# Kernel tuning notes

Measured on AMD Instinct MI355X. Metric: run time of the kernel, lower is better.

The kernel has to match this reference:

```python
import jax, jax.numpy as jnp
import numpy as np

DIM, H, DH = 1024, 16, 64
SCALE = 1.0 / np.sqrt(DH)


def setup_inputs() -> dict:
    key = jax.random.key(0)
    ks = jax.random.split(key, 16)
    B, S = 2, 2048
    glorot = jax.nn.initializers.glorot_uniform()
    def qkv(k):
        return glorot(k, (DIM, H, DH), jnp.float32)
    inp = {
        "x": jax.random.normal(ks[0], (B, S, DIM), jnp.float32),
        "layer_idx": 3,
        "lambda_param": jnp.full((1,), 0.8, jnp.float32),
    }
    for i, br in enumerate(["1", "2"]):
        base = 1 + i * 4
        inp[f"Wq{br}"] = qkv(ks[base])
        inp[f"Wk{br}"] = qkv(ks[base + 1])
        inp[f"Wv{br}"] = qkv(ks[base + 2])
        inp[f"Wo{br}"] = glorot(ks[base + 3], (H, DH, DIM), jnp.float32).reshape(H, DH, DIM)
        inp[f"bq{br}"] = jnp.zeros((H, DH), jnp.float32)
        inp[f"bk{br}"] = jnp.zeros((H, DH), jnp.float32)
        inp[f"bv{br}"] = jnp.zeros((H, DH), jnp.float32)
        inp[f"bo{br}"] = jnp.zeros((DIM,), jnp.float32)
    inp["Wp"] = glorot(ks[9], (DIM, DIM), jnp.float32)
    inp["bp"] = jnp.zeros((DIM,), jnp.float32)
    return inp


def _mha(x, Wq, bq, Wk, bk, Wv, bv, Wo, bo):
    # x: [B,S,D]; per-head projections as in keras.layers.MultiHeadAttention
    q = jnp.einsum("bsd,dhk->bshk", x, Wq) + bq   # [B,S,H,Dh]
    k = jnp.einsum("bsd,dhk->bshk", x, Wk) + bk
    v = jnp.einsum("bsd,dhk->bshk", x, Wv) + bv
    scores = jnp.einsum("bqhd,bkhd->bhqk", q, k) * SCALE  # [B,H,S,S]
    attn = jax.nn.softmax(scores, axis=-1)
    o = jnp.einsum("bhqk,bkhd->bqhd", attn, v)            # [B,S,H,Dh]
    return jnp.einsum("bqhd,hdo->bqo", o, Wo) + bo        # [B,S,D]


def _get_lambda(lambda_param, layer_idx):
    lf = jnp.asarray(layer_idx, jnp.float32)
    exp_term = jnp.exp(-0.3 * jnp.maximum(lf - 1.0, 0.0))
    init = 0.8 - 0.6 * exp_term
    return jnp.clip(init * lambda_param[0], 0.1, 0.9)


def reference(x, layer_idx, lambda_param,
              Wq1, bq1, Wk1, bk1, Wv1, bv1, Wo1, bo1,
              Wq2, bq2, Wk2, bk2, Wv2, bv2, Wo2, bo2,
              Wp, bp):
    a1 = _mha(x, Wq1, bq1, Wk1, bk1, Wv1, bv1, Wo1, bo1)
    a2 = _mha(x, Wq2, bq2, Wk2, bk2, Wv2, bv2, Wo2, bo2)
    lam = _get_lambda(lambda_param, layer_idx)
    diff = a1 - lam * a2
    return diff @ Wp + bp  # dropout is identity at inference
```

## Files before the change

### kernel.cpp

```cpp
#include <hip/hip_runtime.h>
#include <math.h>

typedef unsigned short u16;
typedef __attribute__((ext_vector_type(8))) short bf16x8;
typedef __attribute__((ext_vector_type(4))) float f32x4;
typedef __attribute__((ext_vector_type(4))) unsigned short u16x4;
typedef __attribute__((ext_vector_type(8))) unsigned short u16x8;

constexpr int Sq = 2048, Dm = 1024, Hh = 16, DH = 64;
constexpr int NT = 4096;
constexpr float SEXP = 0.125f * 1.44269504f;

#if __has_builtin(__builtin_amdgcn_exp2f)
#define EXP2(x) __builtin_amdgcn_exp2f(x)
#else
#define EXP2(x) exp2f(x)
#endif

__device__ __forceinline__ u16 f2bf(float f) {
    unsigned u = __float_as_uint(f);
    return (u16)((u + 0x7FFF + ((u >> 16) & 1)) >> 16);
}

__device__ __forceinline__ void async16(u16* lds, const u16* g) {
    __builtin_amdgcn_global_load_lds(
        (const __attribute__((address_space(1))) unsigned int*)g,
        (__attribute__((address_space(3))) unsigned int*)lds, 16, 0, 0);
}

__device__ __forceinline__ float lam_of(const int* lidx, const float* lamp) {
    float lf = (float)lidx[0];
    float init = 0.8f - 0.6f * __expf(-0.3f * fmaxf(lf - 1.0f, 0.0f));
    return fminf(fmaxf(init * lamp[0], 0.1f), 0.9f);
}

__device__ __forceinline__ void gemm_tile_128(
    const u16* __restrict__ A, const u16* __restrict__ Bt, int K,
    int aRow0, int bCol0, u16* As, u16* Bs, f32x4 acc[4][4])
{
    const int tid = threadIdx.x;
    const int w = tid >> 6, lane = tid & 63;
    const int ln = lane & 15, quad = lane >> 4;
    const int wm = (w >> 1) * 64, wn = (w & 1) * 64;
    const int l3 = lane & 7, lr8 = lane >> 3;

    for (int kt = 0; kt < K; kt += 64) {
        __syncthreads();
        #pragma unroll
        for (int c0 = 0; c0 < 4; ++c0) {
            int c = w * 4 + c0;
            int lr = c * 8 + lr8;
            int sc = l3 ^ (lr & 7);
            async16(As + c * 512, A + (size_t)(aRow0 + lr) * K + kt + sc * 8);
            async16(Bs + c * 512, Bt + (size_t)(bCol0 + lr) * K + kt + sc * 8);
        }
        __syncthreads();
        #pragma unroll
        for (int kc = 0; kc < 2; ++kc) {
            bf16x8 af[4], bfr[4];
            #pragma unroll
            for (int mt = 0; mt < 4; ++mt)
                af[mt] = *(const bf16x8*)(As + (wm + mt * 16 + ln) * 64 +
                                          (((kc * 4 + quad) ^ (ln & 7)) * 8));
            #pragma unroll
            for (int nt = 0; nt < 4; ++nt)
                bfr[nt] = *(const bf16x8*)(Bs + (wn + nt * 16 + ln) * 64 +
                                           (((kc * 4 + quad) ^ (ln & 7)) * 8));
            #pragma unroll
            for (int mt = 0; mt < 4; ++mt)
                #pragma unroll
                for (int nt = 0; nt < 4; ++nt)
                    acc[mt][nt] = __builtin_amdgcn_mfma_f32_16x16x32_bf16(
                        af[mt], bfr[nt], acc[mt][nt], 0, 0, 0);
        }
    }
}

__device__ __forceinline__ void gemm_tile_64(
    const u16* __restrict__ A, const u16* __restrict__ Bt, int K,
    int aRow0, int bCol0, u16* As, u16* Bs, f32x4 acc[2][4])
{
    const int tid = threadIdx.x;
    const int w = tid >> 6, lane = tid & 63;
    const int ln = lane & 15, quad = lane >> 4;
    const int wm = (w >> 1) * 32, wn = (w & 1) * 64;
    const int l3 = lane & 7, lr8 = lane >> 3;

    for (int kt = 0; kt < K; kt += 64) {
        __syncthreads();
        #pragma unroll
        for (int c0 = 0; c0 < 2; ++c0) {
            int c = w * 2 + c0;
            int lr = c * 8 + lr8;
            int sc = l3 ^ (lr & 7);
            async16(As + c * 512, A + (size_t)(aRow0 + lr) * K + kt + sc * 8);
        }
        #pragma unroll
        for (int c0 = 0; c0 < 4; ++c0) {
            int c = w * 4 + c0;
            int lr = c * 8 + lr8;
            int sc = l3 ^ (lr & 7);
            async16(Bs + c * 512, Bt + (size_t)(bCol0 + lr) * K + kt + sc * 8);
        }
        __syncthreads();
        #pragma unroll
        for (int kc = 0; kc < 2; ++kc) {
            bf16x8 af[2], bfr[4];
            #pragma unroll
            for (int mt = 0; mt < 2; ++mt)
                af[mt] = *(const bf16x8*)(As + (wm + mt * 16 + ln) * 64 +
                                          (((kc * 4 + quad) ^ (ln & 7)) * 8));
            #pragma unroll
            for (int nt = 0; nt < 4; ++nt)
                bfr[nt] = *(const bf16x8*)(Bs + (wn + nt * 16 + ln) * 64 +
                                           (((kc * 4 + quad) ^ (ln & 7)) * 8));
            #pragma unroll
            for (int mt = 0; mt < 2; ++mt)
                #pragma unroll
                for (int nt = 0; nt < 4; ++nt)
                    acc[mt][nt] = __builtin_amdgcn_mfma_f32_16x16x32_bf16(
                        af[mt], bfr[nt], acc[mt][nt], 0, 0, 0);
        }
    }
}

__global__ __launch_bounds__(256)
void convert_x(const float* __restrict__ x, u16* __restrict__ xb)
{
    int i = (blockIdx.x * 256 + threadIdx.x) * 4;
    float4 v = *(const float4*)(x + i);
    u16x4 o;
    o.x = f2bf(v.x); o.y = f2bf(v.y); o.z = f2bf(v.z); o.w = f2bf(v.w);
    *(u16x4*)(xb + i) = o;
}

struct TcP { const float* src[7]; u16* dst[7]; };

__global__ __launch_bounds__(256)
void wconv(TcP p)
{
    __shared__ float t[64][65];
    const int z = blockIdx.z;
    const float* __restrict__ src = p.src[z];
    u16* __restrict__ dst = p.dst[z];
    const int kb = blockIdx.y * 64, nb = blockIdx.x * 64;
    const int tid = threadIdx.x;
    {
        int r = tid >> 2, cs = (tid & 3) * 16;
        #pragma unroll
        for (int j4 = 0; j4 < 16; j4 += 4) {
            float4 v = *(const float4*)&src[(size_t)(kb + r) * 1024 + nb + cs + j4];
            t[r][cs + j4 + 0] = v.x; t[r][cs + j4 + 1] = v.y;
            t[r][cs + j4 + 2] = v.z; t[r][cs + j4 + 3] = v.w;
        }
    }
    __syncthreads();
    {
        int n = tid >> 2, ks = (tid & 3) * 16;
        u16x8 a, b;
        #pragma unroll
        for (int j = 0; j < 8; ++j) a[j] = f2bf(t[ks + j][n]);
        #pragma unroll
        for (int j = 0; j < 8; ++j) b[j] = f2bf(t[ks + 8 + j][n]);
        u16* o = &dst[(size_t)(nb + n) * 1024 + kb + ks];
        *(u16x8*)o = a;
        *(u16x8*)(o + 8) = b;
    }
}

__global__ __launch_bounds__(256)
void woconv(const float* __restrict__ Wo1, const float* __restrict__ Wo2,
            const float* __restrict__ bo1, const float* __restrict__ bo2,
            const int* __restrict__ lidx, const float* __restrict__ lamp,
            u16* __restrict__ Acat)
{
    const float lam = lam_of(lidx, lamp);
    int i = (blockIdx.x * 256 + threadIdx.x) * 4;
    float4 v;
    if (i < 1048576) {
        v = *(const float4*)(Wo1 + i);
    } else if (i < 2097152) {
        v = *(const float4*)(Wo2 + (i - 1048576));
        v.x *= -lam; v.y *= -lam; v.z *= -lam; v.w *= -lam;
    } else {
        int c = i - 2097152;
        float4 a = *(const float4*)(bo1 + c);
        float4 b = *(const float4*)(bo2 + c);
        v.x = a.x - lam * b.x; v.y = a.y - lam * b.y;
        v.z = a.z - lam * b.z; v.w = a.w - lam * b.w;
    }
    u16x4 o;
    o.x = f2bf(v.x); o.y = f2bf(v.y); o.z = f2bf(v.z); o.w = f2bf(v.w);
    *(u16x4*)(Acat + i) = o;
}

__global__ __launch_bounds__(256, 4)
void wfull_mfma(const u16* __restrict__ Acat, const u16* __restrict__ Wpt,
                const float* __restrict__ bp, u16* __restrict__ Wfull_bt,
                float* __restrict__ bfull)
{
    __shared__ u16 As[64 * 64], Bs[128 * 64];
    const int aRow0 = blockIdx.y * 64, nCol0 = blockIdx.x * 128;
    f32x4 acc[2][4] = {};
    gemm_tile_64(Acat, Wpt, 1024, aRow0, nCol0, As, Bs, acc);

    const int tid = threadIdx.x, w = tid >> 6, lane = tid & 63;
    const int ln = lane & 15, quad = lane >> 4;
    const int wm = (w >> 1) * 32, wn = (w & 1) * 64;
    #pragma unroll
    for (int mt = 0; mt < 2; ++mt) {
        #pragma unroll
        for (int nt = 0; nt < 4; ++nt) {
            int gn = nCol0 + wn + nt * 16 + ln;
            #pragma unroll
            for (int r = 0; r < 4; ++r) {
                int gm = aRow0 + wm + mt * 16 + quad * 4 + r;
                if (gm < 2048)
                    Wfull_bt[(size_t)gn * 2048 + gm] = f2bf(acc[mt][nt][r]);
                else if (gm == 2048)
                    bfull[gn] = acc[mt][nt][r] + bp[gn];
            }
        }
    }
}

struct QkvP { const u16* Wt[6]; const float* bias[6]; u16* out[6]; };

__global__ __launch_bounds__(256, 3)
void qkv_mfma(const u16* __restrict__ xb, QkvP p)
{
    __shared__ u16 As[128 * 64], Bs[128 * 64];
    const int z = blockIdx.z;
    const int type = (z < 3) ? z : z - 3;
    const int aRow0 = blockIdx.y * 128, nCol0 = blockIdx.x * 128;
    f32x4 acc[4][4] = {};
    gemm_tile_128(xb, p.Wt[z], 1024, aRow0, nCol0, As, Bs, acc);

    const float* __restrict__ bias = p.bias[z];
    u16* __restrict__ out = p.out[z];
    const int tid = threadIdx.x, w = tid >> 6, lane = tid & 63;
    const int ln = lane & 15, quad = lane >> 4;
    const int wm = (w >> 1) * 64, wn = (w & 1) * 64;
    #pragma unroll
    for (int mt = 0; mt < 4; ++mt) {
        #pragma unroll
        for (int nt = 0; nt < 4; ++nt) {
            int gn = nCol0 + wn + nt * 16 + ln;
            int h = gn >> 6, dh = gn & 63;
            float bv = bias[gn];
            #pragma unroll
            for (int r = 0; r < 4; ++r) {
                int gm = aRow0 + wm + mt * 16 + quad * 4 + r;
                int b = gm >> 11, s = gm & (Sq - 1);
                size_t bh = (size_t)(b * Hh + h);
                float fv = acc[mt][nt][r] + bv;
                size_t idx;
                u16 val;
                if (type == 0) {
                    val = f2bf(fv * SEXP);
                    idx = bh * 131072 + (size_t)s * 64 + dh;
                } else if (type == 1) {
                    val = f2bf(fv);
                    idx = bh * 131072 + (size_t)(s >> 5) * 2048 +
                          (size_t)((dh >> 5) * 2 + ((s >> 4) & 1)) * 512 +
                          (size_t)(((dh >> 3) & 3) * 16 + (s & 15)) * 8 + (dh & 7);
                } else {
                    val = f2bf(fv);
                    int kidx = ((s & 15) * 2) + ((s >> 4) & 1);
                    idx = bh * 131072 + (size_t)(s >> 5) * 2048 +
                          (size_t)(dh >> 4) * 512 +
                          (size_t)((kidx >> 3) * 16 + (dh & 15)) * 8 + (kidx & 7);
                }
                out[idx] = val;
            }
        }
    }
}

__global__ __launch_bounds__(256, 4)
void attn_mfma(const u16* __restrict__ q1, const u16* __restrict__ kf1,
               const u16* __restrict__ vf1,
               const u16* __restrict__ q2, const u16* __restrict__ kf2,
               const u16* __restrict__ vf2, u16* __restrict__ ocat)
{
    __shared__ __align__(16) char smem[10240];

    const int bh = blockIdx.x, qblk = blockIdx.y, br = blockIdx.z;
    const u16* __restrict__ q  = br ? q2  : q1;
    const u16* __restrict__ kf = br ? kf2 : kf1;
    const u16* __restrict__ vf = br ? vf2 : vf1;

    const int tid = threadIdx.x, w = tid >> 6, lane = tid & 63;
    const int ln = lane & 15, quad = lane >> 4;
    char* Pbase = smem + w * 2560;

    const u16* qbase = q + (size_t)bh * 131072 +
                       (size_t)(qblk * 128 + w * 32) * 64;
    bf16x8 qf[2][2];
    #pragma unroll
    for (int mt = 0; mt < 2; ++mt)
        #pragma unroll
        for (int kc = 0; kc < 2; ++kc)
            qf[mt][kc] = *(const bf16x8*)(qbase + (mt * 16 + ln) * 64 +
                                          kc * 32 + quad * 8);

    bf16x8 ones;
    #pragma unroll
    for (int j = 0; j < 8; ++j) ones[j] = (short)0x3F80;
    const f32x4 zero4 = {0.f, 0.f, 0.f, 0.f};

    f32x4 oacc[2][4] = {};
    f32x4 lacc[2] = {};

    const u16* kbase = kf + (size_t)bh * 131072 + lane * 8;
    const u16* vbase = vf + (size_t)bh * 131072 + lane * 8;

    for (int it = 0; it < 32; ++it) {
        #pragma unroll
        for (int u = 0; u < 2; ++u) {
            const int kt = it * 2 + u;
            const u16* kp = kbase + (size_t)kt * 2048;
            const u16* vp = vbase + (size_t)kt * 2048;

            bf16x8 kfr[2][2];
            #pragma unroll
            for (int kc = 0; kc < 2; ++kc)
                #pragma unroll
                for (int nt = 0; nt < 2; ++nt)
                    kfr[nt][kc] = *(const bf16x8*)(kp + (kc * 2 + nt) * 512);

            f32x4 sacc[2][2];
            #pragma unroll
            for (int mt = 0; mt < 2; ++mt)
                #pragma unroll
                for (int nt = 0; nt < 2; ++nt)
                    sacc[mt][nt] = __builtin_amdgcn_mfma_f32_16x16x32_bf16(
                        qf[mt][0], kfr[nt][0], zero4, 0, 0, 0);
            #pragma unroll
            for (int mt = 0; mt < 2; ++mt)
                #pragma unroll
                for (int nt = 0; nt < 2; ++nt)
                    sacc[mt][nt] = __builtin_amdgcn_mfma_f32_16x16x32_bf16(
                        qf[mt][1], kfr[nt][1], sacc[mt][nt], 0, 0, 0);

            #pragma unroll
            for (int mt = 0; mt < 2; ++mt) {
                #pragma unroll
                for (int r = 0; r < 4; ++r) {
                    float p0 = EXP2(sacc[mt][0][r]);
                    float p1 = EXP2(sacc[mt][1][r]);
                    unsigned a  = __float_as_uint(p0) + 0x8000u;
                    unsigned b2 = __float_as_uint(p1) + 0x8000u;
                    unsigned pk = __builtin_amdgcn_perm(b2, a, 0x07060302);
                    int row = mt * 16 + quad * 4 + r;
                    *(unsigned*)(Pbase + row * 80 + (((ln >> 2) ^ r) << 4) +
                                 ((ln & 3) << 2)) = pk;
                }
            }

            bf16x8 vfr[4];
            #pragma unroll
            for (int dt = 0; dt < 4; ++dt)
                vfr[dt] = *(const bf16x8*)(vp + dt * 512);

            #pragma unroll
            for (int mt = 0; mt < 2; ++mt) {
                bf16x8 pf = *(const bf16x8*)(Pbase + (mt * 16 + ln) * 80 +
                                             ((quad ^ (ln & 3)) << 4));
                lacc[mt] = __builtin_amdgcn_mfma_f32_16x16x32_bf16(
                    pf, ones, lacc[mt], 0, 0, 0);
                #pragma unroll
                for (int dt = 0; dt < 4; ++dt)
                    oacc[mt][dt] = __builtin_amdgcn_mfma_f32_16x16x32_bf16(
                        pf, vfr[dt], oacc[mt][dt], 0, 0, 0);
            }
        }
        __builtin_amdgcn_s_barrier();
    }

    const int b = bh >> 4, h = bh & 15;
    #pragma unroll
    for (int mt = 0; mt < 2; ++mt) {
        #pragma unroll
        for (int r = 0; r < 4; ++r) {
            float inv = 1.0f / lacc[mt][r];
            int s = qblk * 128 + w * 32 + mt * 16 + quad * 4 + r;
            size_t rowb = (size_t)(b * Sq + s) * 2048 + br * 1024 + h * 64;
            #pragma unroll
            for (int dt = 0; dt < 4; ++dt)
                ocat[rowb + dt * 16 + ln] = f2bf(oacc[mt][dt][r] * inv);
        }
    }
}

__global__ __launch_bounds__(256, 4)
void out_mfma(const u16* __restrict__ ocat, const u16* __restrict__ Wfull_bt,
              const float* __restrict__ bfull, float* __restrict__ outb)
{
    __shared__ u16 As[64 * 64], Bs[128 * 64];
    const int aRow0 = blockIdx.y * 64, nCol0 = blockIdx.x * 128;
    f32x4 acc[2][4] = {};
    gemm_tile_64(ocat, Wfull_bt, 2048, aRow0, nCol0, As, Bs, acc);

    const int tid = threadIdx.x, w = tid >> 6, lane = tid & 63;
    const int ln = lane & 15, quad = lane >> 4;
    const int wm = (w >> 1) * 32, wn = (w & 1) * 64;
    #pragma unroll
    for (int mt = 0; mt < 2; ++mt) {
        #pragma unroll
        for (int nt = 0; nt < 4; ++nt) {
            int gn = nCol0 + wn + nt * 16 + ln;
            float bv = bfull[gn];
            #pragma unroll
            for (int r = 0; r < 4; ++r) {
                int gm = aRow0 + wm + mt * 16 + quad * 4 + r;
                outb[(size_t)gm * 1024 + gn] = acc[mt][nt][r] + bv;
            }
        }
    }
}

extern "C" void kernel_launch(void* const* d_in, const int* in_sizes, int n_in,
                              void* d_out, int out_size, void* d_ws, size_t ws_size,
                              hipStream_t stream)
{
    const float* x    = (const float*)d_in[0];
    const int*   lidx = (const int*)  d_in[1];
    const float* lamp = (const float*)d_in[2];
    const float* Wq1  = (const float*)d_in[3];
    const float* Wk1  = (const float*)d_in[4];
    const float* Wv1  = (const float*)d_in[5];
    const float* Wo1  = (const float*)d_in[6];
    const float* bq1  = (const float*)d_in[7];
    const float* bk1  = (const float*)d_in[8];
    const float* bv1  = (const float*)d_in[9];
    const float* bo1  = (const float*)d_in[10];
    const float* Wq2  = (const float*)d_in[11];
    const float* Wk2  = (const float*)d_in[12];
    const float* Wv2  = (const float*)d_in[13];
    const float* Wo2  = (const float*)d_in[14];
    const float* bq2  = (const float*)d_in[15];
    const float* bk2  = (const float*)d_in[16];
    const float* bv2  = (const float*)d_in[17];
    const float* bo2  = (const float*)d_in[18];
    const float* Wp   = (const float*)d_in[19];
    const float* bp   = (const float*)d_in[20];

    char* wsb = (char*)d_ws;
    const size_t MB = 1 << 20;
    u16* xb    = (u16*)(wsb + 0 * MB);
    u16* Wt0   = (u16*)(wsb + 8 * MB);
    u16* Wpt   = (u16*)(wsb + 20 * MB);
    u16* Acat  = (u16*)(wsb + 22 * MB);
    u16* Wfull = (u16*)(wsb + 27 * MB);
    float* bfull = (float*)(wsb + 31 * MB);
    u16* qb1   = (u16*)(wsb + 32 * MB);
    u16* kb1   = (u16*)(wsb + 40 * MB);
    u16* vb1   = (u16*)(wsb + 48 * MB);
    u16* qb2   = (u16*)(wsb + 56 * MB);
    u16* kb2   = (u16*)(wsb + 64 * MB);
    u16* vb2   = (u16*)(wsb + 72 * MB);
    u16* ocat  = (u16*)(wsb + 80 * MB);

    convert_x<<<dim3(NT * Dm / 1024), dim3(256), 0, stream>>>(x, xb);

    TcP tp;
    const float* wsrc[7] = {Wq1, Wk1, Wv1, Wq2, Wk2, Wv2, Wp};
    for (int i = 0; i < 7; ++i) tp.src[i] = wsrc[i];
    for (int i = 0; i < 6; ++i) tp.dst[i] = Wt0 + (size_t)i * 1024 * 1024;
    tp.dst[6] = Wpt;
    wconv<<<dim3(16, 16, 7), dim3(256), 0, stream>>>(tp);

    woconv<<<dim3(2049), dim3(256), 0, stream>>>(
        Wo1, Wo2, bo1, bo2, lidx, lamp, Acat);

    wfull_mfma<<<dim3(8, 33), dim3(256), 0, stream>>>(
        Acat, Wpt, bp, Wfull, bfull);

    QkvP qp;
    qp.Wt[0] = Wt0 + 0 * 1048576; qp.bias[0] = bq1; qp.out[0] = qb1;
    qp.Wt[1] = Wt0 + 1 * 1048576; qp.bias[1] = bk1; qp.out[1] = kb1;
    qp.Wt[2] = Wt0 + 2 * 1048576; qp.bias[2] = bv1; qp.out[2] = vb1;
    qp.Wt[3] = Wt0 + 3 * 1048576; qp.bias[3] = bq2; qp.out[3] = qb2;
    qp.Wt[4] = Wt0 + 4 * 1048576; qp.bias[4] = bk2; qp.out[4] = kb2;
    qp.Wt[5] = Wt0 + 5 * 1048576; qp.bias[5] = bv2; qp.out[5] = vb2;
    qkv_mfma<<<dim3(8, 32, 6), dim3(256), 0, stream>>>(xb, qp);

    attn_mfma<<<dim3(32, 16, 2), dim3(256), 0, stream>>>(
        qb1, kb1, vb1, qb2, kb2, vb2, ocat);

    out_mfma<<<dim3(8, 64), dim3(256), 0, stream>>>(
        ocat, Wfull, bfull, (float*)d_out);
}
```

Baseline: 330.5 us.

## Double-buffer GEMM tiles, merge prep and GEMM launches, raise MFMA priority

The 128-wide GEMM tile loop now double-buffers its LDS tiles, issuing async loads for the next K-slice while the current one is multiplied. The three prep kernels are merged into one launch, and the Wfull and QKV GEMMs into a single gemms launch selected by blockIdx.z. The attention kernel wraps its MFMA sections in s_setprio(1)/s_setprio(0). These changes aim to cut launch overhead and load latency, at the cost of more LDS per block (64KB shared buffer, launch bounds of 2) and some idle blocks in the merged grid.

```diff
diff --git a/kernel.cpp b/kernel.cpp
--- a/kernel.cpp
+++ b/kernel.cpp
@@ -44,27 +44,43 @@
     const int wm = (w >> 1) * 64, wn = (w & 1) * 64;
     const int l3 = lane & 7, lr8 = lane >> 3;
 
+    #pragma unroll
+    for (int c0 = 0; c0 < 4; ++c0) {
+        int c = w * 4 + c0;
+        int lr = c * 8 + lr8;
+        int sc = l3 ^ (lr & 7);
+        async16(As + c * 512, A + (size_t)(aRow0 + lr) * K + sc * 8);
+        async16(Bs + c * 512, Bt + (size_t)(bCol0 + lr) * K + sc * 8);
+    }
+    __syncthreads();
+
+    int cur = 0;
     for (int kt = 0; kt < K; kt += 64) {
-        __syncthreads();
-        #pragma unroll
-        for (int c0 = 0; c0 < 4; ++c0) {
-            int c = w * 4 + c0;
-            int lr = c * 8 + lr8;
-            int sc = l3 ^ (lr & 7);
-            async16(As + c * 512, A + (size_t)(aRow0 + lr) * K + kt + sc * 8);
-            async16(Bs + c * 512, Bt + (size_t)(bCol0 + lr) * K + kt + sc * 8);
-        }
-        __syncthreads();
+        const int ktn = kt + 64;
+        if (ktn < K) {
+            u16* Asn = As + (cur ^ 1) * 8192;
+            u16* Bsn = Bs + (cur ^ 1) * 8192;
+            #pragma unroll
+            for (int c0 = 0; c0 < 4; ++c0) {
+                int c = w * 4 + c0;
+                int lr = c * 8 + lr8;
+                int sc = l3 ^ (lr & 7);
+                async16(Asn + c * 512, A + (size_t)(aRow0 + lr) * K + ktn + sc * 8);
+                async16(Bsn + c * 512, Bt + (size_t)(bCol0 + lr) * K + ktn + sc * 8);
+            }
+        }
+        const u16* Asc = As + cur * 8192;
+        const u16* Bsc = Bs + cur * 8192;
         #pragma unroll
         for (int kc = 0; kc < 2; ++kc) {
             bf16x8 af[4], bfr[4];
             #pragma unroll
             for (int mt = 0; mt < 4; ++mt)
-                af[mt] = *(const bf16x8*)(As + (wm + mt * 16 + ln) * 64 +
+                af[mt] = *(const bf16x8*)(Asc + (wm + mt * 16 + ln) * 64 +
                                           (((kc * 4 + quad) ^ (ln & 7)) * 8));
             #pragma unroll
             for (int nt = 0; nt < 4; ++nt)
-                bfr[nt] = *(const bf16x8*)(Bs + (wn + nt * 16 + ln) * 64 +
+                bfr[nt] = *(const bf16x8*)(Bsc + (wn + nt * 16 + ln) * 64 +
                                            (((kc * 4 + quad) ^ (ln & 7)) * 8));
             #pragma unroll
             for (int mt = 0; mt < 4; ++mt)
@@ -73,6 +89,8 @@
                     acc[mt][nt] = __builtin_amdgcn_mfma_f32_16x16x32_bf16(
                         af[mt], bfr[nt], acc[mt][nt], 0, 0, 0);
         }
+        __syncthreads();
+        cur ^= 1;
     }
 }
 
@@ -124,122 +142,130 @@
     }
 }
 
+struct PrepP {
+    const float* x; u16* xb;
+    const float* wsrc[7]; u16* wdst[7];
+    const float* Wo1; const float* Wo2;
+    const float* bo1; const float* bo2;
+    const int* lidx; const float* lamp;
+    u16* Acat;
+};
+
 __global__ __launch_bounds__(256)
-void convert_x(const float* __restrict__ x, u16* __restrict__ xb)
-{
-    int i = (blockIdx.x * 256 + threadIdx.x) * 4;
-    float4 v = *(const float4*)(x + i);
-    u16x4 o;
-    o.x = f2bf(v.x); o.y = f2bf(v.y); o.z = f2bf(v.z); o.w = f2bf(v.w);
-    *(u16x4*)(xb + i) = o;
-}
-
-struct TcP { const float* src[7]; u16* dst[7]; };
-
-__global__ __launch_bounds__(256)
-void wconv(TcP p)
+void prep(PrepP p)
 {
     __shared__ float t[64][65];
+    int b = blockIdx.x;
+    const int tid = threadIdx.x;
+
+    if (b < 4096) {
+        int i = (b * 256 + tid) * 4;
+        float4 v = *(const float4*)(p.x + i);
+        u16x4 o;
+        o.x = f2bf(v.x); o.y = f2bf(v.y); o.z = f2bf(v.z); o.w = f2bf(v.w);
+        *(u16x4*)(p.xb + i) = o;
+        return;
+    }
+    b -= 4096;
+    if (b < 1792) {
+        int z = b >> 8;
+        int rem = b & 255;
+        const float* __restrict__ src = p.wsrc[z];
+        u16* __restrict__ dst = p.wdst[z];
+        const int kb = (rem >> 4) * 64, nb = (rem & 15) * 64;
+        {
+            int r = tid >> 2, cs = (tid & 3) * 16;
+            #pragma unroll
+            for (int j4 = 0; j4 < 16; j4 += 4) {
+                float4 v = *(const float4*)&src[(size_t)(kb + r) * 1024 + nb + cs + j4];
+                t[r][cs + j4 + 0] = v.x; t[r][cs + j4 + 1] = v.y;
+                t[r][cs + j4 + 2] = v.z; t[r][cs + j4 + 3] = v.w;
+            }
+        }
+        __syncthreads();
+        {
+            int n = tid >> 2, ks = (tid & 3) * 16;
+            u16x8 a2, b2;
+            #pragma unroll
+            for (int j = 0; j < 8; ++j) a2[j] = f2bf(t[ks + j][n]);
+            #pragma unroll
+            for (int j = 0; j < 8; ++j) b2[j] = f2bf(t[ks + 8 + j][n]);
+            u16* o = &dst[(size_t)(nb + n) * 1024 + kb + ks];
+            *(u16x8*)o = a2;
+            *(u16x8*)(o + 8) = b2;
+        }
+        return;
+    }
+    b -= 1792;
+    {
+        const float lam = lam_of(p.lidx, p.lamp);
+        int i = (b * 256 + tid) * 4;
+        float4 v;
+        if (i < 1048576) {
+            v = *(const float4*)(p.Wo1 + i);
+        } else if (i < 2097152) {
+            v = *(const float4*)(p.Wo2 + (i - 1048576));
+            v.x *= -lam; v.y *= -lam; v.z *= -lam; v.w *= -lam;
+        } else {
+            int c = i - 2097152;
+            float4 a = *(const float4*)(p.bo1 + c);
+            float4 b2 = *(const float4*)(p.bo2 + c);
+            v.x = a.x - lam * b2.x; v.y = a.y - lam * b2.y;
+            v.z = a.z - lam * b2.z; v.w = a.w - lam * b2.w;
+        }
+        u16x4 o;
+        o.x = f2bf(v.x); o.y = f2bf(v.y); o.z = f2bf(v.z); o.w = f2bf(v.w);
+        *(u16x4*)(p.Acat + i) = o;
+    }
+}
+
+struct GemmP {
+    const u16* xb;
+    const u16* Wt[6]; const float* bias[6]; u16* out[6];
+    const u16* Acat; const u16* Wpt; const float* bp;
+    u16* Wfull_bt; float* bfull;
+};
+
+__global__ __launch_bounds__(256, 2)
+void gemms(GemmP p)
+{
+    __shared__ u16 smem[32768];
     const int z = blockIdx.z;
-    const float* __restrict__ src = p.src[z];
-    u16* __restrict__ dst = p.dst[z];
-    const int kb = blockIdx.y * 64, nb = blockIdx.x * 64;
-    const int tid = threadIdx.x;
-    {
-        int r = tid >> 2, cs = (tid & 3) * 16;
-        #pragma unroll
-        for (int j4 = 0; j4 < 16; j4 += 4) {
-            float4 v = *(const float4*)&src[(size_t)(kb + r) * 1024 + nb + cs + j4];
-            t[r][cs + j4 + 0] = v.x; t[r][cs + j4 + 1] = v.y;
-            t[r][cs + j4 + 2] = v.z; t[r][cs + j4 + 3] = v.w;
-        }
-    }
-    __syncthreads();
-    {
-        int n = tid >> 2, ks = (tid & 3) * 16;
-        u16x8 a, b;
-        #pragma unroll
-        for (int j = 0; j < 8; ++j) a[j] = f2bf(t[ks + j][n]);
-        #pragma unroll
-        for (int j = 0; j < 8; ++j) b[j] = f2bf(t[ks + 8 + j][n]);
-        u16* o = &dst[(size_t)(nb + n) * 1024 + kb + ks];
-        *(u16x8*)o = a;
-        *(u16x8*)(o + 8) = b;
-    }
-}
-
-__global__ __launch_bounds__(256)
-void woconv(const float* __restrict__ Wo1, const float* __restrict__ Wo2,
-            const float* __restrict__ bo1, const float* __restrict__ bo2,
-            const int* __restrict__ lidx, const float* __restrict__ lamp,
-            u16* __restrict__ Acat)
-{
-    const float lam = lam_of(lidx, lamp);
-    int i = (blockIdx.x * 256 + threadIdx.x) * 4;
-    float4 v;
-    if (i < 1048576) {
-        v = *(const float4*)(Wo1 + i);
-    } else if (i < 2097152) {
-        v = *(const float4*)(Wo2 + (i - 1048576));
-        v.x *= -lam; v.y *= -lam; v.z *= -lam; v.w *= -lam;
-    } else {
-        int c = i - 2097152;
-        float4 a = *(const float4*)(bo1 + c);
-        float4 b = *(const float4*)(bo2 + c);
-        v.x = a.x - lam * b.x; v.y = a.y - lam * b.y;
-        v.z = a.z - lam * b.z; v.w = a.w - lam * b.w;
-    }
-    u16x4 o;
-    o.x = f2bf(v.x); o.y = f2bf(v.y); o.z = f2bf(v.z); o.w = f2bf(v.w);
-    *(u16x4*)(Acat + i) = o;
-}
-
-__global__ __launch_bounds__(256, 4)
-void wfull_mfma(const u16* __restrict__ Acat, const u16* __restrict__ Wpt,
-                const float* __restrict__ bp, u16* __restrict__ Wfull_bt,
-                float* __restrict__ bfull)
-{
-    __shared__ u16 As[64 * 64], Bs[128 * 64];
-    const int aRow0 = blockIdx.y * 64, nCol0 = blockIdx.x * 128;
-    f32x4 acc[2][4] = {};
-    gemm_tile_64(Acat, Wpt, 1024, aRow0, nCol0, As, Bs, acc);
-
     const int tid = threadIdx.x, w = tid >> 6, lane = tid & 63;
     const int ln = lane & 15, quad = lane >> 4;
-    const int wm = (w >> 1) * 32, wn = (w & 1) * 64;
-    #pragma unroll
-    for (int mt = 0; mt < 2; ++mt) {
-        #pragma unroll
-        for (int nt = 0; nt < 4; ++nt) {
-            int gn = nCol0 + wn + nt * 16 + ln;
-            #pragma unroll
-            for (int r = 0; r < 4; ++r) {
-                int gm = aRow0 + wm + mt * 16 + quad * 4 + r;
-                if (gm < 2048)
-                    Wfull_bt[(size_t)gn * 2048 + gm] = f2bf(acc[mt][nt][r]);
-                else if (gm == 2048)
-                    bfull[gn] = acc[mt][nt][r] + bp[gn];
-            }
-        }
-    }
-}
-
-struct QkvP { const u16* Wt[6]; const float* bias[6]; u16* out[6]; };
-
-__global__ __launch_bounds__(256, 3)
-void qkv_mfma(const u16* __restrict__ xb, QkvP p)
-{
-    __shared__ u16 As[128 * 64], Bs[128 * 64];
-    const int z = blockIdx.z;
+
+    if (z == 6) {
+        const int aRow0 = blockIdx.y * 64, nCol0 = blockIdx.x * 128;
+        f32x4 acc[2][4] = {};
+        gemm_tile_64(p.Acat, p.Wpt, 1024, aRow0, nCol0, smem, smem + 4096, acc);
+
+        const int wm = (w >> 1) * 32, wn = (w & 1) * 64;
+        #pragma unroll
+        for (int mt = 0; mt < 2; ++mt) {
+            #pragma unroll
+            for (int nt = 0; nt < 4; ++nt) {
+                int gn = nCol0 + wn + nt * 16 + ln;
+                #pragma unroll
+                for (int r = 0; r < 4; ++r) {
+                    int gm = aRow0 + wm + mt * 16 + quad * 4 + r;
+                    if (gm < 2048)
+                        p.Wfull_bt[(size_t)gn * 2048 + gm] = f2bf(acc[mt][nt][r]);
+                    else if (gm == 2048)
+                        p.bfull[gn] = acc[mt][nt][r] + p.bp[gn];
+                }
+            }
+        }
+        return;
+    }
+    if (blockIdx.y >= 32) return;
+
     const int type = (z < 3) ? z : z - 3;
     const int aRow0 = blockIdx.y * 128, nCol0 = blockIdx.x * 128;
     f32x4 acc[4][4] = {};
-    gemm_tile_128(xb, p.Wt[z], 1024, aRow0, nCol0, As, Bs, acc);
+    gemm_tile_128(p.xb, p.Wt[z], 1024, aRow0, nCol0, smem, smem + 16384, acc);
 
     const float* __restrict__ bias = p.bias[z];
     u16* __restrict__ out = p.out[z];
-    const int tid = threadIdx.x, w = tid >> 6, lane = tid & 63;
-    const int ln = lane & 15, quad = lane >> 4;
     const int wm = (w >> 1) * 64, wn = (w & 1) * 64;
     #pragma unroll
     for (int mt = 0; mt < 4; ++mt) {
@@ -329,6 +355,7 @@
                 for (int nt = 0; nt < 2; ++nt)
                     kfr[nt][kc] = *(const bf16x8*)(kp + (kc * 2 + nt) * 512);
 
+            __builtin_amdgcn_s_setprio(1);
             f32x4 sacc[2][2];
             #pragma unroll
             for (int mt = 0; mt < 2; ++mt)
@@ -342,6 +369,7 @@
                 for (int nt = 0; nt < 2; ++nt)
                     sacc[mt][nt] = __builtin_amdgcn_mfma_f32_16x16x32_bf16(
                         qf[mt][1], kfr[nt][1], sacc[mt][nt], 0, 0, 0);
+            __builtin_amdgcn_s_setprio(0);
 
             #pragma unroll
             for (int mt = 0; mt < 2; ++mt) {
@@ -363,6 +391,7 @@
             for (int dt = 0; dt < 4; ++dt)
                 vfr[dt] = *(const bf16x8*)(vp + dt * 512);
 
+            __builtin_amdgcn_s_setprio(1);
             #pragma unroll
             for (int mt = 0; mt < 2; ++mt) {
                 bf16x8 pf = *(const bf16x8*)(Pbase + (mt * 16 + ln) * 80 +
@@ -374,6 +403,7 @@
                     oacc[mt][dt] = __builtin_amdgcn_mfma_f32_16x16x32_bf16(
                         pf, vfr[dt], oacc[mt][dt], 0, 0, 0);
             }
+            __builtin_amdgcn_s_setprio(0);
         }
         __builtin_amdgcn_s_barrier();
     }
@@ -462,29 +492,27 @@
     u16* vb2   = (u16*)(wsb + 72 * MB);
     u16* ocat  = (u16*)(wsb + 80 * MB);
 
-    convert_x<<<dim3(NT * Dm / 1024), dim3(256), 0, stream>>>(x, xb);
-
-    TcP tp;
+    PrepP pp;
+    pp.x = x; pp.xb = xb;
     const float* wsrc[7] = {Wq1, Wk1, Wv1, Wq2, Wk2, Wv2, Wp};
-    for (int i = 0; i < 7; ++i) tp.src[i] = wsrc[i];
-    for (int i = 0; i < 6; ++i) tp.dst[i] = Wt0 + (size_t)i * 1024 * 1024;
-    tp.dst[6] = Wpt;
-    wconv<<<dim3(16, 16, 7), dim3(256), 0, stream>>>(tp);
-
-    woconv<<<dim3(2049), dim3(256), 0, stream>>>(
-        Wo1, Wo2, bo1, bo2, lidx, lamp, Acat);
-
-    wfull_mfma<<<dim3(8, 33), dim3(256), 0, stream>>>(
-        Acat, Wpt, bp, Wfull, bfull);
-
-    QkvP qp;
-    qp.Wt[0] = Wt0 + 0 * 1048576; qp.bias[0] = bq1; qp.out[0] = qb1;
-    qp.Wt[1] = Wt0 + 1 * 1048576; qp.bias[1] = bk1; qp.out[1] = kb1;
-    qp.Wt[2] = Wt0 + 2 * 1048576; qp.bias[2] = bv1; qp.out[2] = vb1;
-    qp.Wt[3] = Wt0 + 3 * 1048576; qp.bias[3] = bq2; qp.out[3] = qb2;
-    qp.Wt[4] = Wt0 + 4 * 1048576; qp.bias[4] = bk2; qp.out[4] = kb2;
-    qp.Wt[5] = Wt0 + 5 * 1048576; qp.bias[5] = bv2; qp.out[5] = vb2;
-    qkv_mfma<<<dim3(8, 32, 6), dim3(256), 0, stream>>>(xb, qp);
+    for (int i = 0; i < 7; ++i) pp.wsrc[i] = wsrc[i];
+    for (int i = 0; i < 6; ++i) pp.wdst[i] = Wt0 + (size_t)i * 1024 * 1024;
+    pp.wdst[6] = Wpt;
+    pp.Wo1 = Wo1; pp.Wo2 = Wo2; pp.bo1 = bo1; pp.bo2 = bo2;
+    pp.lidx = lidx; pp.lamp = lamp; pp.Acat = Acat;
+    prep<<<dim3(4096 + 1792 + 2049), dim3(256), 0, stream>>>(pp);
+
+    GemmP gp;
+    gp.xb = xb;
+    gp.Wt[0] = Wt0 + 0 * 1048576; gp.bias[0] = bq1; gp.out[0] = qb1;
+    gp.Wt[1] = Wt0 + 1 * 1048576; gp.bias[1] = bk1; gp.out[1] = kb1;
+    gp.Wt[2] = Wt0 + 2 * 1048576; gp.bias[2] = bv1; gp.out[2] = vb1;
+    gp.Wt[3] = Wt0 + 3 * 1048576; gp.bias[3] = bq2; gp.out[3] = qb2;
+    gp.Wt[4] = Wt0 + 4 * 1048576; gp.bias[4] = bk2; gp.out[4] = kb2;
+    gp.Wt[5] = Wt0 + 5 * 1048576; gp.bias[5] = bv2; gp.out[5] = vb2;
+    gp.Acat = Acat; gp.Wpt = Wpt; gp.bp = bp;
+    gp.Wfull_bt = Wfull; gp.bfull = bfull;
+    gemms<<<dim3(8, 33, 7), dim3(256), 0, stream>>>(gp);
 
     attn_mfma<<<dim3(32, 16, 2), dim3(256), 0, stream>>>(
         qb1, kb1, vb1, qb2, kb2, vb2, ocat);
```

Result: faster. 318.6 us (-3.6%).
